# Optimization experiments

Hardware: AMD Instinct MI355X
Metric: run time of the kernel (lower is better)

The kernel has to match this reference:

```python
import jax, jax.numpy as jnp
import numpy as np

B, S, E, H = 4, 2048, 1024, 16
D = E // H  # head_dim = 64

def setup_inputs() -> dict:
    key = jax.random.key(0)
    k1, k2, k3, k4, k5 = jax.random.split(key, 5)
    x = jax.random.normal(k1, (B, S, E), dtype=jnp.float32)
    # causal mask, broadcast over batch and heads; mask==0 -> -inf
    mask = jnp.tril(jnp.ones((S, S), dtype=jnp.int32))[None, None, :, :]
    Wqkv = jax.random.normal(k2, (E, 3 * E), dtype=jnp.float32) * (1.0 / np.sqrt(E))
    bqkv = jax.random.normal(k3, (3 * E,), dtype=jnp.float32) * 0.02
    Wo = jax.random.normal(k4, (E, E), dtype=jnp.float32) * (1.0 / np.sqrt(E))
    bo = jax.random.normal(k5, (E,), dtype=jnp.float32) * 0.02
    return {"x": x, "mask": mask, "Wqkv": Wqkv, "bqkv": bqkv, "Wo": Wo, "bo": bo}

def reference(x, mask, Wqkv, bqkv, Wo, bo):
    b, s, e = x.shape
    scale = 1.0 / np.sqrt(D)
    qkv = x @ Wqkv + bqkv                      # [b,s,3e]
    qkv = qkv.reshape(b, s, H, 3 * D).transpose(0, 2, 1, 3)  # [b,h,s,3d]
    q, k, v = jnp.split(qkv, 3, axis=-1)       # each [b,h,s,d]
    scores = jnp.einsum('bnqd,bnkd->bnqk', q, k) * scale
    scores = jnp.where(mask == 0, -jnp.inf, scores)
    probs = jax.nn.softmax(scores, axis=-1)
    attn = jnp.einsum('bnqk,bnkd->bnqd', probs, v)  # [b,h,s,d]
    # Faithful to source: reshape (b,h,s,d) -> (b,s,e) WITHOUT transposing back
    attn = attn.reshape(b, s, e)
    return attn @ Wo + bo
```

## Files before the change

kernel.cpp:

```cpp
#include <hip/hip_runtime.h>

typedef __attribute__((ext_vector_type(8))) short bf16x8;
typedef __attribute__((ext_vector_type(4))) float f32x4;
typedef __attribute__((ext_vector_type(2))) unsigned int u32x2;
typedef __attribute__((ext_vector_type(4))) unsigned int u32x4;

#define MFMA16(a, b, c) __builtin_amdgcn_mfma_f32_16x16x32_bf16((a), (b), (c), 0, 0, 0)

#define S_LEN 2048
#define NHEAD 16
#define DHEAD 64
#define BH    64
#define MROWS 8192

__device__ __forceinline__ unsigned short f2bf(float f) {
  unsigned int u = __builtin_bit_cast(unsigned int, f);
  u += 0x7FFFu + ((u >> 16) & 1u);
  return (unsigned short)(u >> 16);
}

__device__ __forceinline__ void gl_lds16(const void* g, void* l) {
  __builtin_amdgcn_global_load_lds(
      (const __attribute__((address_space(1))) void*)g,
      (__attribute__((address_space(3))) void*)l, 16, 0, 0);
}

__device__ __forceinline__ unsigned int pkbf(float lo, float hi) {
  unsigned int ulo = __builtin_bit_cast(unsigned int, lo) + 0x8000u;
  unsigned int uhi = __builtin_bit_cast(unsigned int, hi) + 0x8000u;
  return __builtin_amdgcn_perm(uhi, ulo, 0x07060302u);
}

__global__ __launch_bounds__(256) void cast_bf16(const float* __restrict__ src,
                                                 unsigned short* __restrict__ dst, int n) {
  int i = (blockIdx.x * 256 + threadIdx.x) * 4;
  if (i + 3 < n) {
    f32x4 v = *(const f32x4*)(src + i);
    unsigned long long pk =
        (unsigned long long)f2bf(v[0]) |
        ((unsigned long long)f2bf(v[1]) << 16) |
        ((unsigned long long)f2bf(v[2]) << 32) |
        ((unsigned long long)f2bf(v[3]) << 48);
    *(unsigned long long*)(dst + i) = pk;
  }
}

__global__ __launch_bounds__(256) void transpose_cast(const float* __restrict__ src,
                                                      unsigned short* __restrict__ dst,
                                                      int R, int C) {
  __shared__ float tile[32][33];
  int c0 = blockIdx.x * 32, r0 = blockIdx.y * 32;
  int tx = threadIdx.x, ty = threadIdx.y;
  for (int i = 0; i < 32; i += 8)
    tile[ty + i][tx] = src[(size_t)(r0 + ty + i) * C + c0 + tx];
  __syncthreads();
  for (int i = 0; i < 32; i += 8)
    dst[(size_t)(c0 + ty + i) * R + r0 + tx] = f2bf(tile[tx][ty + i]);
}

__global__ __launch_bounds__(256) void transpose_cast_qkv(const float* __restrict__ src,
                                                          unsigned short* __restrict__ dst) {
  __shared__ float tile[32][33];
  int c0 = blockIdx.x * 32, r0 = blockIdx.y * 32;
  int tx = threadIdx.x, ty = threadIdx.y;
  for (int i = 0; i < 32; i += 8)
    tile[ty + i][tx] = src[(size_t)(r0 + ty + i) * 3072 + c0 + tx];
  __syncthreads();
  for (int i = 0; i < 32; i += 8) {
    int oc = c0 + ty + i;
    int h = oc / 192, rr = oc % 192;
    int nc = ((rr >> 6) << 10) + (h << 6) + (rr & 63);
    dst[(size_t)nc * 1024 + r0 + tx] = f2bf(tile[tx][ty + i]);
  }
}

#define GEMM_CORE(A_, Bt_)                                                              \
  __shared__ unsigned short As[128 * 32];                                               \
  __shared__ unsigned short Bs[128 * 32];                                               \
  const int tid = threadIdx.x;                                                          \
  const int w = tid >> 6, lane = tid & 63, l15 = lane & 15, quad = lane >> 4;           \
  const int wm = w >> 1, wn = w & 1;                                                    \
  const int col0 = blockIdx.x * 128, row0 = blockIdx.y * 128;                           \
  f32x4 acc[4][4] = {};                                                                 \
  for (int kt = 0; kt < 32; ++kt) {                                                     \
    const int k0 = kt * 32;                                                             \
    for (int p = 0; p < 2; ++p) {                                                       \
      int c = p * 256 + tid;                                                            \
      int m = c >> 2, k8 = (c & 3) * 8;                                                 \
      void* ldsA = (char*)As + (size_t)(p * 256 + (tid & 192)) * 16;                    \
      void* ldsB = (char*)Bs + (size_t)(p * 256 + (tid & 192)) * 16;                    \
      gl_lds16(A_ + (size_t)(row0 + m) * 1024 + k0 + k8, ldsA);                         \
      gl_lds16(Bt_ + (size_t)(col0 + m) * 1024 + k0 + k8, ldsB);                        \
    }                                                                                   \
    __syncthreads();                                                                    \
    bf16x8 af[4], bfr[4];                                                               \
    for (int i = 0; i < 4; ++i)                                                         \
      af[i] = *(const bf16x8*)&As[(wm * 64 + i * 16 + l15) * 32 + quad * 8];            \
    for (int j = 0; j < 4; ++j)                                                         \
      bfr[j] = *(const bf16x8*)&Bs[(wn * 64 + j * 16 + l15) * 32 + quad * 8];           \
    for (int i = 0; i < 4; ++i)                                                         \
      for (int j = 0; j < 4; ++j)                                                       \
        acc[i][j] = MFMA16(af[i], bfr[j], acc[i][j]);                                   \
    __syncthreads();                                                                    \
  }

__global__ __launch_bounds__(256) void gemm_qkv(const unsigned short* __restrict__ A,
                                                const unsigned short* __restrict__ Bt,
                                                const float* __restrict__ bias,
                                                unsigned short* __restrict__ Qb,
                                                unsigned short* __restrict__ Kb,
                                                unsigned short* __restrict__ Vtb) {
  __shared__ float Es[4][16][66];
  GEMM_CORE(A, Bt)
  const int bx = col0 >> 7;
  float bv[4];
  #pragma unroll
  for (int j = 0; j < 4; ++j) {
    int nc = col0 + wn * 64 + j * 16 + l15;
    int oc = ((nc >> 6) & 15) * 192 + (nc >> 10) * 64 + (nc & 63);
    bv[j] = bias[oc];
  }
  const float sc = (bx < 8) ? 0.18033688011112042f : 1.0f;
  const int b = row0 >> 11;
  const int srow0 = (row0 & 2047) + wm * 64;
  const int h = ((col0 + wn * 64) >> 6) & 15;
  float (*Ew)[66] = Es[w];

  if (bx < 16) {
    const int lr = lane >> 2, ch2 = lane & 3, d0 = ch2 * 16;
    unsigned short* base = (bx < 8 ? Qb : Kb) + ((size_t)(b * 16 + h) * 2048) * 64;
    for (int i = 0; i < 4; ++i) {
      #pragma unroll
      for (int j = 0; j < 4; ++j)
        #pragma unroll
        for (int r = 0; r < 4; ++r)
          Ew[quad * 4 + r][j * 16 + l15] = (acc[i][j][r] + bv[j]) * sc;
      float v[16];
      #pragma unroll
      for (int c = 0; c < 4; ++c)
        *(f32x4*)&v[4 * c] = *(const f32x4*)&Ew[lr][d0 + 4 * c];
      u32x4 pk0 = {pkbf(v[0], v[1]), pkbf(v[2], v[3]), pkbf(v[4], v[5]), pkbf(v[6], v[7])};
      u32x4 pk1 = {pkbf(v[8], v[9]), pkbf(v[10], v[11]), pkbf(v[12], v[13]), pkbf(v[14], v[15])};
      unsigned short* dst = base + (size_t)(srow0 + i * 16 + lr) * 64 + d0;
      *(u32x4*)dst = pk0;
      *(u32x4*)(dst + 8) = pk1;
    }
  } else {
    const int d = lane;
    unsigned short* base = Vtb + ((size_t)(b * 16 + h) * 64 + d) * 2048;
    for (int i = 0; i < 4; ++i) {
      #pragma unroll
      for (int j = 0; j < 4; ++j)
        #pragma unroll
        for (int r = 0; r < 4; ++r)
          Ew[quad * 4 + r][j * 16 + l15] = acc[i][j][r] + bv[j];
      float e[16];
      #pragma unroll
      for (int k = 0; k < 16; ++k) e[k] = Ew[k][d];
      u32x4 pk0 = {pkbf(e[0], e[1]), pkbf(e[2], e[3]), pkbf(e[4], e[5]), pkbf(e[6], e[7])};
      u32x4 pk1 = {pkbf(e[8], e[9]), pkbf(e[10], e[11]), pkbf(e[12], e[13]), pkbf(e[14], e[15])};
      unsigned short* dst = base + srow0 + i * 16;
      *(u32x4*)dst = pk0;
      *(u32x4*)(dst + 8) = pk1;
    }
  }
}

__global__ __launch_bounds__(256) void gemm_out(const unsigned short* __restrict__ A,
                                                const unsigned short* __restrict__ Bt,
                                                const float* __restrict__ bias,
                                                float* __restrict__ out) {
  GEMM_CORE(A, Bt)
  for (int i = 0; i < 4; ++i) {
    int grow = row0 + wm * 64 + i * 16 + quad * 4;
    for (int j = 0; j < 4; ++j) {
      int gcol = col0 + wn * 64 + j * 16 + l15;
      float bvv = bias[gcol];
      for (int r = 0; r < 4; ++r)
        out[(size_t)(grow + r) * 1024 + gcol] = acc[i][j][r] + bvv;
    }
  }
}

__global__ __launch_bounds__(256) void attn_kernel(const unsigned short* __restrict__ Qb,
                                                   const unsigned short* __restrict__ Kb,
                                                   const unsigned short* __restrict__ Vtb,
                                                   unsigned short* __restrict__ attnout) {
  __shared__ unsigned short K0[64 * 32], K1[64 * 32];
  __shared__ unsigned short V0[64 * 32], V1[64 * 32];
  __shared__ unsigned short P0[4][4][512], P1[4][4][512];
  __shared__ float Lbc[4][64];

  const int tid = threadIdx.x;
  const int w = tid >> 6, lane = tid & 63, l15 = lane & 15, quad = lane >> 4;
  const int i2 = blockIdx.x >> 6;
  const int jj = ((i2 & 1) << 1) | ((i2 >> 1) & 1);
  const int qt = (i2 & 4) ? jj : 7 - jj;
  const int bh = blockIdx.x & 63;
  const int q0w = qt * 256 + w * 64;

  const unsigned short* Qg = Qb + (size_t)bh * S_LEN * DHEAD;
  const unsigned short* Kg = Kb + (size_t)bh * S_LEN * DHEAD;
  const unsigned short* Vg = Vtb + (size_t)bh * DHEAD * S_LEN;

  bf16x8 qf[4][2];
  #pragma unroll
  for (int sub = 0; sub < 4; ++sub) {
    const unsigned short* p = Qg + (size_t)(q0w + sub * 16 + l15) * DHEAD + quad * 8;
    qf[sub][0] = *(const bf16x8*)p;
    qf[sub][1] = *(const bf16x8*)(p + 32);
  }

  const int srow = tid >> 2, sc8 = (tid & 3) * 8;
  const unsigned short* kgb = Kg + srow * 64 + sc8;
  const unsigned short* vgb = Vg + (size_t)srow * S_LEN + sc8;
  const int wKo = srow * 32 + sc8;

  const int psw = (l15 & 3) ^ ((l15 >> 2) & 3);
  const int pw0 = l15 * 32 + (((quad >> 1) ^ psw) << 3) + ((quad & 1) << 2);
  const int pw1 = l15 * 32 + ((((quad >> 1) + 2) ^ psw) << 3) + ((quad & 1) << 2);
  const int pro = l15 * 32 + ((quad ^ psw) << 3);
  const int kvo = l15 * 32 + quad * 8;

  f32x4 oacc[4][4] = {};
  float lacc[4] = {0.f, 0.f, 0.f, 0.f};

  const int ktdiag = 4 * qt;
  const int nkt = ktdiag + 4;

  bf16x8 kr0 = *(const bf16x8*)kgb, kr1 = *(const bf16x8*)(kgb + 32);
  bf16x8 vr0 = *(const bf16x8*)vgb, vr1 = *(const bf16x8*)(vgb + 32);

  for (int kt = 0; kt < nkt; ++kt) {
    *(bf16x8*)&K0[wKo] = kr0;  *(bf16x8*)&K1[wKo] = kr1;
    *(bf16x8*)&V0[wKo] = vr0;  *(bf16x8*)&V1[wKo] = vr1;
    __syncthreads();
    if (kt + 1 < nkt) {
      const unsigned short* kp = kgb + (kt + 1) * 4096;
      const unsigned short* vp = vgb + (kt + 1) * 64;
      kr0 = *(const bf16x8*)kp;  kr1 = *(const bf16x8*)(kp + 32);
      vr0 = *(const bf16x8*)vp;  vr1 = *(const bf16x8*)(vp + 32);
    }

    const int t = kt - ktdiag;
    const bool act = (t < 0) || (w >= t);

    if (act) {
      if (t < 0) {
        #pragma unroll
        for (int jk = 0; jk < 4; ++jk) {
          bf16x8 kf0 = *(const bf16x8*)&K0[jk * 512 + kvo];
          bf16x8 kf1 = *(const bf16x8*)&K1[jk * 512 + kvo];
          #pragma unroll
          for (int sub = 0; sub < 4; ++sub) {
            f32x4 z = {};
            z = MFMA16(kf0, qf[sub][0], z);
            z = MFMA16(kf1, qf[sub][1], z);
            float e0 = __builtin_amdgcn_exp2f(z[0]);
            float e1 = __builtin_amdgcn_exp2f(z[1]);
            float e2 = __builtin_amdgcn_exp2f(z[2]);
            float e3 = __builtin_amdgcn_exp2f(z[3]);
            lacc[sub] += (e0 + e1) + (e2 + e3);
            unsigned short* pd = (jk < 2) ? P0[w][sub] : P1[w][sub];
            *(u32x2*)&pd[(jk & 1) ? pw1 : pw0] = (u32x2){pkbf(e0, e1), pkbf(e2, e3)};
          }
        }
      } else {
        const bool dg = (t == w);
        #pragma unroll
        for (int jk = 0; jk < 4; ++jk) {
          bf16x8 kf0 = *(const bf16x8*)&K0[jk * 512 + kvo];
          bf16x8 kf1 = *(const bf16x8*)&K1[jk * 512 + kvo];
          #pragma unroll
          for (int sub = 0; sub < 4; ++sub) {
            unsigned short* pd = (jk < 2) ? P0[w][sub] : P1[w][sub];
            unsigned int* dst = (unsigned int*)&pd[(jk & 1) ? pw1 : pw0];
            if (dg && jk > sub) { *(u32x2*)dst = (u32x2){0u, 0u}; continue; }
            f32x4 z = {};
            z = MFMA16(kf0, qf[sub][0], z);
            z = MFMA16(kf1, qf[sub][1], z);
            if (dg && jk == sub) {
              #pragma unroll
              for (int r = 0; r < 4; ++r)
                if (quad * 4 + r > l15) z[r] = -3e38f;
            }
            float e0 = __builtin_amdgcn_exp2f(z[0]);
            float e1 = __builtin_amdgcn_exp2f(z[1]);
            float e2 = __builtin_amdgcn_exp2f(z[2]);
            float e3 = __builtin_amdgcn_exp2f(z[3]);
            lacc[sub] += (e0 + e1) + (e2 + e3);
            *(u32x2*)dst = (u32x2){pkbf(e0, e1), pkbf(e2, e3)};
          }
        }
      }

      bf16x8 pf[4][2];
      #pragma unroll
      for (int sub = 0; sub < 4; ++sub) {
        pf[sub][0] = *(const bf16x8*)&P0[w][sub][pro];
        pf[sub][1] = *(const bf16x8*)&P1[w][sub][pro];
      }
      #pragma unroll
      for (int dt = 0; dt < 4; ++dt) {
        bf16x8 vb0 = *(const bf16x8*)&V0[dt * 512 + kvo];
        bf16x8 vb1 = *(const bf16x8*)&V1[dt * 512 + kvo];
        #pragma unroll
        for (int sub = 0; sub < 4; ++sub) {
          oacc[sub][dt] = MFMA16(pf[sub][0], vb0, oacc[sub][dt]);
          oacc[sub][dt] = MFMA16(pf[sub][1], vb1, oacc[sub][dt]);
        }
      }
    }
    __syncthreads();
  }

  #pragma unroll
  for (int sub = 0; sub < 4; ++sub) {
    float l = lacc[sub];
    l += __shfl_xor(l, 16);
    l += __shfl_xor(l, 32);
    if (quad == 0) Lbc[w][sub * 16 + l15] = l;
  }
  #pragma unroll
  for (int sub = 0; sub < 4; ++sub) {
    f32x4 l4 = *(const f32x4*)&Lbc[w][sub * 16 + quad * 4];
    int qbase = q0w + sub * 16 + quad * 4;
    unsigned short* dst = attnout + ((size_t)bh * S_LEN + qbase) * DHEAD;
    #pragma unroll
    for (int r = 0; r < 4; ++r) {
      float inv = __builtin_amdgcn_rcpf(l4[r]);
      #pragma unroll
      for (int dt = 0; dt < 4; ++dt)
        dst[(size_t)r * DHEAD + dt * 16 + l15] = f2bf(oacc[sub][dt][r] * inv);
    }
  }
}

extern "C" void kernel_launch(void* const* d_in, const int* in_sizes, int n_in,
                              void* d_out, int out_size, void* d_ws, size_t ws_size,
                              hipStream_t stream) {
  const float* x    = (const float*)d_in[0];
  const float* Wqkv = (const float*)d_in[2];
  const float* bqkv = (const float*)d_in[3];
  const float* Wo   = (const float*)d_in[4];
  const float* bo   = (const float*)d_in[5];
  float* out = (float*)d_out;

  char* ws = (char*)d_ws;
  unsigned short* Xbf   = (unsigned short*)(ws);
  unsigned short* WqkvT = (unsigned short*)(ws + 16777216);
  unsigned short* WoT   = (unsigned short*)(ws + 23068672);
  unsigned short* Qb    = (unsigned short*)(ws + 25165824);
  unsigned short* Kb    = (unsigned short*)(ws + 41943040);
  unsigned short* Vtb   = (unsigned short*)(ws + 58720256);
  unsigned short* Attn  = (unsigned short*)(ws + 75497472);

  cast_bf16<<<8192, 256, 0, stream>>>(x, Xbf, MROWS * 1024);
  transpose_cast_qkv<<<dim3(96, 32), dim3(32, 8), 0, stream>>>(Wqkv, WqkvT);
  transpose_cast<<<dim3(32, 32), dim3(32, 8), 0, stream>>>(Wo, WoT, 1024, 1024);
  gemm_qkv<<<dim3(24, 64), 256, 0, stream>>>(Xbf, WqkvT, bqkv, Qb, Kb, Vtb);
  attn_kernel<<<512, 256, 0, stream>>>(Qb, Kb, Vtb, Attn);
  gemm_out<<<dim3(8, 64), 256, 0, stream>>>(Attn, WoT, bo, out);
}
```

Baseline: 266.4 us.

## Rewrite QKV GEMM with 256x256 tiles, double-buffered async LDS staging, swizzling

Replaces the QKV projection GEMM with a 512-thread, 256x256-tile kernel. It double-buffers the global-to-LDS loads across K tiles, with explicit vmcnt/lgkmcnt waits, barriers and raised MFMA priority, so loads overlap the matrix math. The LDS layout is XOR-swizzled to avoid bank conflicts, and the grid is remapped to a 1D grid of 384 blocks with a block-index permutation for better L2 reuse. This adds 128KB of LDS per block and relies on hand-tuned wait counts, which trades occupancy and fragility for higher MFMA utilisation in the dominant GEMM.

```diff
diff --git a/kernel.cpp b/kernel.cpp
--- a/kernel.cpp
+++ b/kernel.cpp
@@ -104,15 +104,155 @@
     __syncthreads();                                                                    \
   }
 
-__global__ __launch_bounds__(256) void gemm_qkv(const unsigned short* __restrict__ A,
-                                                const unsigned short* __restrict__ Bt,
-                                                const float* __restrict__ bias,
-                                                unsigned short* __restrict__ Qb,
-                                                unsigned short* __restrict__ Kb,
-                                                unsigned short* __restrict__ Vtb) {
-  __shared__ float Es[4][16][66];
-  GEMM_CORE(A, Bt)
-  const int bx = col0 >> 7;
+
+#define VM6 asm volatile("s_waitcnt vmcnt(6)" ::: "memory")
+#define VM0 asm volatile("s_waitcnt vmcnt(0)" ::: "memory")
+#define LGKM0 asm volatile("s_waitcnt lgkmcnt(0)" ::: "memory")
+#define BAR __builtin_amdgcn_s_barrier()
+
+#define STAGE_A(KT, H)                                                           \
+  do {                                                                           \
+    char* lb_ = SHB + (((KT) & 1) * 65536 + (H) * 16384) + stgo;                 \
+    const unsigned short* gs_ = a_src + (KT) * 64 + (H) * 32;                    \
+    gl_lds16(gs_, lb_);                                                          \
+    gl_lds16(gs_ + 131072, lb_ + 8192);                                          \
+  } while (0)
+#define STAGE_B(KT, H)                                                           \
+  do {                                                                           \
+    char* lb_ = SHB + (((KT) & 1) * 65536 + 32768 + (H) * 16384) + stgo;         \
+    const unsigned short* gs_ = b_src + (KT) * 64 + (H) * 32;                    \
+    gl_lds16(gs_, lb_);                                                          \
+    gl_lds16(gs_ + 131072, lb_ + 8192);                                          \
+  } while (0)
+
+#define MFMA_BLOCK(MH)                                                           \
+  __builtin_amdgcn_s_setprio(1);                                                 \
+  acc[(MH)*4+0][0] = MFMA16(af0, bq0, acc[(MH)*4+0][0]);                         \
+  acc[(MH)*4+0][1] = MFMA16(af0, bq1, acc[(MH)*4+0][1]);                         \
+  acc[(MH)*4+0][2] = MFMA16(af0, bq2, acc[(MH)*4+0][2]);                         \
+  acc[(MH)*4+0][3] = MFMA16(af0, bq3, acc[(MH)*4+0][3]);                         \
+  acc[(MH)*4+1][0] = MFMA16(af1, bq0, acc[(MH)*4+1][0]);                         \
+  acc[(MH)*4+1][1] = MFMA16(af1, bq1, acc[(MH)*4+1][1]);                         \
+  acc[(MH)*4+1][2] = MFMA16(af1, bq2, acc[(MH)*4+1][2]);                         \
+  acc[(MH)*4+1][3] = MFMA16(af1, bq3, acc[(MH)*4+1][3]);                         \
+  acc[(MH)*4+2][0] = MFMA16(af2, bq0, acc[(MH)*4+2][0]);                         \
+  acc[(MH)*4+2][1] = MFMA16(af2, bq1, acc[(MH)*4+2][1]);                         \
+  acc[(MH)*4+2][2] = MFMA16(af2, bq2, acc[(MH)*4+2][2]);                         \
+  acc[(MH)*4+2][3] = MFMA16(af2, bq3, acc[(MH)*4+2][3]);                         \
+  acc[(MH)*4+3][0] = MFMA16(af3, bq0, acc[(MH)*4+3][0]);                         \
+  acc[(MH)*4+3][1] = MFMA16(af3, bq1, acc[(MH)*4+3][1]);                         \
+  acc[(MH)*4+3][2] = MFMA16(af3, bq2, acc[(MH)*4+3][2]);                         \
+  acc[(MH)*4+3][3] = MFMA16(af3, bq3, acc[(MH)*4+3][3]);                         \
+  __builtin_amdgcn_s_setprio(0)
+
+#define KTILE(BUF, JT, G0, G2, VMW)                                              \
+  {                                                                              \
+    {                                                    \
+      const char* Ah_ = SHB + (BUF) * 65536;                                     \
+      const char* Bh_ = SHB + (BUF) * 65536 + 32768;                             \
+      bf16x8 af0 = *(const bf16x8*)(Ah_ + abase);                                \
+      bf16x8 af1 = *(const bf16x8*)(Ah_ + abase + 1024);                         \
+      bf16x8 af2 = *(const bf16x8*)(Ah_ + abase + 2048);                         \
+      bf16x8 af3 = *(const bf16x8*)(Ah_ + abase + 3072);                         \
+      bq0 = *(const bf16x8*)(Bh_ + bbase);                                       \
+      bq1 = *(const bf16x8*)(Bh_ + bbase + 1024);                                \
+      bq2 = *(const bf16x8*)(Bh_ + bbase + 2048);                                \
+      bq3 = *(const bf16x8*)(Bh_ + bbase + 3072);                                \
+      if (G0) STAGE_B((JT) + 1, 1);                                              \
+      BAR;                                                                       \
+      LGKM0;                                                                     \
+      MFMA_BLOCK(0);                                                             \
+      BAR;                                                                       \
+    }                                                                            \
+    {                                                    \
+      const char* Ah_ = SHB + (BUF) * 65536;                                     \
+      bf16x8 af0 = *(const bf16x8*)(Ah_ + abase + 4096);                         \
+      bf16x8 af1 = *(const bf16x8*)(Ah_ + abase + 5120);                         \
+      bf16x8 af2 = *(const bf16x8*)(Ah_ + abase + 6144);                         \
+      bf16x8 af3 = *(const bf16x8*)(Ah_ + abase + 7168);                         \
+      BAR;                                                                       \
+      if (G2) STAGE_A((JT) + 2, 0);                                              \
+      LGKM0;                                                                     \
+      MFMA_BLOCK(1);                                                             \
+      BAR;                                                                       \
+    }                                                                            \
+    {                                                    \
+      const char* Ah_ = SHB + (BUF) * 65536 + 16384;                             \
+      const char* Bh_ = SHB + (BUF) * 65536 + 32768 + 16384;                     \
+      bf16x8 af0 = *(const bf16x8*)(Ah_ + abase);                                \
+      bf16x8 af1 = *(const bf16x8*)(Ah_ + abase + 1024);                         \
+      bf16x8 af2 = *(const bf16x8*)(Ah_ + abase + 2048);                         \
+      bf16x8 af3 = *(const bf16x8*)(Ah_ + abase + 3072);                         \
+      bq0 = *(const bf16x8*)(Bh_ + bbase);                                       \
+      bq1 = *(const bf16x8*)(Bh_ + bbase + 1024);                                \
+      bq2 = *(const bf16x8*)(Bh_ + bbase + 2048);                                \
+      bq3 = *(const bf16x8*)(Bh_ + bbase + 3072);                                \
+      if (G2) STAGE_B((JT) + 2, 0);                                              \
+      BAR;                                                                       \
+      LGKM0;                                                                     \
+      MFMA_BLOCK(0);                                                             \
+      BAR;                                                                       \
+    }                                                                            \
+    {                                                    \
+      const char* Ah_ = SHB + (BUF) * 65536 + 16384;                             \
+      bf16x8 af0 = *(const bf16x8*)(Ah_ + abase + 4096);                         \
+      bf16x8 af1 = *(const bf16x8*)(Ah_ + abase + 5120);                         \
+      bf16x8 af2 = *(const bf16x8*)(Ah_ + abase + 6144);                         \
+      bf16x8 af3 = *(const bf16x8*)(Ah_ + abase + 7168);                         \
+      BAR;                                                                       \
+      if (G2) STAGE_A((JT) + 2, 1);                                              \
+      LGKM0;                                                                     \
+      MFMA_BLOCK(1);                                                             \
+      VMW;                                                                       \
+      BAR;                                                                       \
+    }                                                                            \
+  }
+
+__global__ __launch_bounds__(512, 2) void gemm_qkv(const unsigned short* __restrict__ A,
+                                                   const unsigned short* __restrict__ Bt,
+                                                   const float* __restrict__ bias,
+                                                   unsigned short* __restrict__ Qb,
+                                                   unsigned short* __restrict__ Kb,
+                                                   unsigned short* __restrict__ Vtb) {
+  __shared__ unsigned short SH[65536];
+  char* SHB = (char*)SH;
+  const int tid = threadIdx.x;
+  const int w = tid >> 6, lane = tid & 63, l15 = lane & 15, quad = lane >> 4;
+  const int wm = w >> 2, wn = w & 3;
+  const int g = ((blockIdx.x & 7) * 48) + (blockIdx.x >> 3);
+  const int bx = g % 12, by = g / 12;
+  const int col0 = bx << 8, row0 = by << 8;
+
+  const int qa = quad ^ ((l15 >> 1) & 3);
+  const int abase = (wm * 128 + l15) * 64 + qa * 16;
+  const int bbase = (wn * 64 + l15) * 64 + qa * 16;
+
+  const int qsw = (tid & 3) ^ ((tid >> 3) & 3);
+  const unsigned short* a_src = A + (size_t)(row0 + (tid >> 2)) * 1024 + qsw * 8;
+  const unsigned short* b_src = Bt + (size_t)(col0 + (tid >> 2)) * 1024 + qsw * 8;
+  const int stgo = (tid & ~63) * 16;
+
+  f32x4 acc[8][4] = {};
+  bf16x8 bq0, bq1, bq2, bq3;
+
+  STAGE_A(0, 0); STAGE_B(0, 0); STAGE_A(0, 1); STAGE_B(0, 1);
+  STAGE_A(1, 0); STAGE_B(1, 0); STAGE_A(1, 1);
+  VM6;
+  BAR;
+
+  #pragma unroll 1
+  for (int jj = 0; jj < 8; ++jj) {
+    const int j0 = jj * 2;
+    const bool more = (jj < 7);
+    KTILE(0, j0, 1, more, { if (more) VM6; else VM0; })
+    KTILE(1, j0 + 1, more, more, { if (more) VM6; })
+  }
+  __syncthreads();
+
+  const int which = col0 >> 10;
+  const int h = ((col0 + wn * 64) >> 6) & 15;
+  const int b = row0 >> 11;
+  const int srow0 = (row0 & 2047) + wm * 128;
   float bv[4];
   #pragma unroll
   for (int j = 0; j < 4; ++j) {
@@ -120,46 +260,45 @@
     int oc = ((nc >> 6) & 15) * 192 + (nc >> 10) * 64 + (nc & 63);
     bv[j] = bias[oc];
   }
-  const float sc = (bx < 8) ? 0.18033688011112042f : 1.0f;
-  const int b = row0 >> 11;
-  const int srow0 = (row0 & 2047) + wm * 64;
-  const int h = ((col0 + wn * 64) >> 6) & 15;
-  float (*Ew)[66] = Es[w];
-
-  if (bx < 16) {
-    const int lr = lane >> 2, ch2 = lane & 3, d0 = ch2 * 16;
-    unsigned short* base = (bx < 8 ? Qb : Kb) + ((size_t)(b * 16 + h) * 2048) * 64;
-    for (int i = 0; i < 4; ++i) {
+  float* Ew = (float*)SHB + w * 1072;
+
+  if (which < 2) {
+    const float sc = (which == 0) ? 0.18033688011112042f : 1.0f;
+    const int lr = lane >> 2, d0 = (lane & 3) * 16;
+    unsigned short* base = (which == 0 ? Qb : Kb) + ((size_t)(b * 16 + h) * 2048 + srow0) * 64;
+    #pragma unroll
+    for (int i = 0; i < 8; ++i) {
       #pragma unroll
       for (int j = 0; j < 4; ++j)
         #pragma unroll
         for (int r = 0; r < 4; ++r)
-          Ew[quad * 4 + r][j * 16 + l15] = (acc[i][j][r] + bv[j]) * sc;
+          Ew[(quad * 4 + r) * 66 + j * 16 + l15] = (acc[i][j][r] + bv[j]) * sc;
       float v[16];
       #pragma unroll
       for (int c = 0; c < 4; ++c)
-        *(f32x4*)&v[4 * c] = *(const f32x4*)&Ew[lr][d0 + 4 * c];
+        *(f32x4*)&v[4 * c] = *(const f32x4*)&Ew[lr * 66 + d0 + 4 * c];
       u32x4 pk0 = {pkbf(v[0], v[1]), pkbf(v[2], v[3]), pkbf(v[4], v[5]), pkbf(v[6], v[7])};
       u32x4 pk1 = {pkbf(v[8], v[9]), pkbf(v[10], v[11]), pkbf(v[12], v[13]), pkbf(v[14], v[15])};
-      unsigned short* dst = base + (size_t)(srow0 + i * 16 + lr) * 64 + d0;
+      unsigned short* dst = base + (size_t)(i * 16 + lr) * 64 + d0;
       *(u32x4*)dst = pk0;
       *(u32x4*)(dst + 8) = pk1;
     }
   } else {
     const int d = lane;
-    unsigned short* base = Vtb + ((size_t)(b * 16 + h) * 64 + d) * 2048;
-    for (int i = 0; i < 4; ++i) {
+    unsigned short* base = Vtb + ((size_t)(b * 16 + h) * 64 + d) * 2048 + srow0;
+    #pragma unroll
+    for (int i = 0; i < 8; ++i) {
       #pragma unroll
       for (int j = 0; j < 4; ++j)
         #pragma unroll
         for (int r = 0; r < 4; ++r)
-          Ew[quad * 4 + r][j * 16 + l15] = acc[i][j][r] + bv[j];
+          Ew[(quad * 4 + r) * 66 + j * 16 + l15] = acc[i][j][r] + bv[j];
       float e[16];
       #pragma unroll
-      for (int k = 0; k < 16; ++k) e[k] = Ew[k][d];
+      for (int k = 0; k < 16; ++k) e[k] = Ew[k * 66 + d];
       u32x4 pk0 = {pkbf(e[0], e[1]), pkbf(e[2], e[3]), pkbf(e[4], e[5]), pkbf(e[6], e[7])};
       u32x4 pk1 = {pkbf(e[8], e[9]), pkbf(e[10], e[11]), pkbf(e[12], e[13]), pkbf(e[14], e[15])};
-      unsigned short* dst = base + srow0 + i * 16;
+      unsigned short* dst = base + i * 16;
       *(u32x4*)dst = pk0;
       *(u32x4*)(dst + 8) = pk1;
     }
@@ -358,7 +497,7 @@
   cast_bf16<<<8192, 256, 0, stream>>>(x, Xbf, MROWS * 1024);
   transpose_cast_qkv<<<dim3(96, 32), dim3(32, 8), 0, stream>>>(Wqkv, WqkvT);
   transpose_cast<<<dim3(32, 32), dim3(32, 8), 0, stream>>>(Wo, WoT, 1024, 1024);
-  gemm_qkv<<<dim3(24, 64), 256, 0, stream>>>(Xbf, WqkvT, bqkv, Qb, Kb, Vtb);
+  gemm_qkv<<<384, 512, 0, stream>>>(Xbf, WqkvT, bqkv, Qb, Kb, Vtb);
   attn_kernel<<<512, 256, 0, stream>>>(Qb, Kb, Vtb, Attn);
   gemm_out<<<dim3(8, 64), 256, 0, stream>>>(Attn, WoT, bo, out);
 }
```

New measurement: 271.5 us. About the same (+1.9%).

## Rewrite QKV GEMM as 256x256 tile, double-buffered, software-pipelined kernel

Applied to the files above, without the earlier changes.

Replaces the simple 128x128 QKV projection GEMM with a 512-thread, 256x256-tile kernel. It double-buffers K=64 slabs in 128KB of LDS with direct global-to-LDS loads, interleaves the loads with MFMA blocks using explicit vmcnt waits, barriers and setprio, swizzles the LDS layout to avoid bank conflicts, and remaps the block index for L2 locality. The goal is to hide memory latency and raise MFMA utilization in the largest GEMM. The cost is high register pressure and only one block per CU because of the LDS use. The epilogue reuses the staging LDS.

```diff
diff --git a/kernel.cpp b/kernel.cpp
--- a/kernel.cpp
+++ b/kernel.cpp
@@ -101,18 +101,138 @@
     for (int i = 0; i < 4; ++i)                                                         \
       for (int j = 0; j < 4; ++j)                                                       \
         acc[i][j] = MFMA16(af[i], bfr[j], acc[i][j]);                                   \
+    for (int __z = 0; __z < 1; ++__z) ;                                                 \
     __syncthreads();                                                                    \
   }
 
-__global__ __launch_bounds__(256) void gemm_qkv(const unsigned short* __restrict__ A,
-                                                const unsigned short* __restrict__ Bt,
-                                                const float* __restrict__ bias,
-                                                unsigned short* __restrict__ Qb,
-                                                unsigned short* __restrict__ Kb,
-                                                unsigned short* __restrict__ Vtb) {
-  __shared__ float Es[4][16][66];
-  GEMM_CORE(A, Bt)
-  const int bx = col0 >> 7;
+
+#define VM8 asm volatile("s_waitcnt vmcnt(8)" ::: "memory")
+#define VM6 asm volatile("s_waitcnt vmcnt(6)" ::: "memory")
+#define VM4 asm volatile("s_waitcnt vmcnt(4)" ::: "memory")
+#define VM0 asm volatile("s_waitcnt vmcnt(0)" ::: "memory")
+#define VMNOP ((void)0)
+#define BAR __builtin_amdgcn_s_barrier()
+#define SB  __builtin_amdgcn_sched_barrier(0)
+
+#define STAGE_A(KT, H)                                                           \
+  do {                                                                           \
+    char* lb_ = SHB + (((KT) & 1) * 65536 + (H) * 16384) + stgo;                 \
+    const unsigned short* gs_ = a_src + (KT) * 64 + (H) * 32;                    \
+    gl_lds16(gs_, lb_);                                                          \
+    gl_lds16(gs_ + 131072, lb_ + 8192);                                          \
+  } while (0)
+#define STAGE_B(KT, H)                                                           \
+  do {                                                                           \
+    char* lb_ = SHB + (((KT) & 1) * 65536 + 32768 + (H) * 16384) + stgo;         \
+    const unsigned short* gs_ = b_src + (KT) * 64 + (H) * 32;                    \
+    gl_lds16(gs_, lb_);                                                          \
+    gl_lds16(gs_ + 131072, lb_ + 8192);                                          \
+  } while (0)
+
+#define MFMA_BLK(A0,A1,A2,A3, B0,B1,B2,B3, MH)                                   \
+  __builtin_amdgcn_s_setprio(1);                                                 \
+  acc[(MH)*4+0][0] = MFMA16(A0, B0, acc[(MH)*4+0][0]);                           \
+  acc[(MH)*4+0][1] = MFMA16(A0, B1, acc[(MH)*4+0][1]);                           \
+  acc[(MH)*4+0][2] = MFMA16(A0, B2, acc[(MH)*4+0][2]);                           \
+  acc[(MH)*4+0][3] = MFMA16(A0, B3, acc[(MH)*4+0][3]);                           \
+  acc[(MH)*4+1][0] = MFMA16(A1, B0, acc[(MH)*4+1][0]);                           \
+  acc[(MH)*4+1][1] = MFMA16(A1, B1, acc[(MH)*4+1][1]);                           \
+  acc[(MH)*4+1][2] = MFMA16(A1, B2, acc[(MH)*4+1][2]);                           \
+  acc[(MH)*4+1][3] = MFMA16(A1, B3, acc[(MH)*4+1][3]);                           \
+  acc[(MH)*4+2][0] = MFMA16(A2, B0, acc[(MH)*4+2][0]);                           \
+  acc[(MH)*4+2][1] = MFMA16(A2, B1, acc[(MH)*4+2][1]);                           \
+  acc[(MH)*4+2][2] = MFMA16(A2, B2, acc[(MH)*4+2][2]);                           \
+  acc[(MH)*4+2][3] = MFMA16(A2, B3, acc[(MH)*4+2][3]);                           \
+  acc[(MH)*4+3][0] = MFMA16(A3, B0, acc[(MH)*4+3][0]);                           \
+  acc[(MH)*4+3][1] = MFMA16(A3, B1, acc[(MH)*4+3][1]);                           \
+  acc[(MH)*4+3][2] = MFMA16(A3, B2, acc[(MH)*4+3][2]);                           \
+  acc[(MH)*4+3][3] = MFMA16(A3, B3, acc[(MH)*4+3][3]);                           \
+  __builtin_amdgcn_s_setprio(0)
+
+#define RD4(D0,D1,D2,D3, P)                                                      \
+  D0 = *(const bf16x8*)((P));                                                    \
+  D1 = *(const bf16x8*)((P) + 1024);                                             \
+  D2 = *(const bf16x8*)((P) + 2048);                                             \
+  D3 = *(const bf16x8*)((P) + 3072)
+
+#define KT1(BUF, JT, G1, G2, RDN, VMA_, VMB_)                                    \
+  {              \
+    if (G1) { STAGE_A((JT)+1, 1); STAGE_B((JT)+1, 1); }                          \
+    MFMA_BLK(afA0,afA1,afA2,afA3, bqA0,bqA1,bqA2,bqA3, 0);                       \
+    RD4(afB0,afB1,afB2,afB3, SHB + (BUF)*65536 + abase + 4096);                  \
+    VMA_; SB; BAR; SB;                                                           \
+  }                                                                              \
+  {                 \
+    MFMA_BLK(afB0,afB1,afB2,afB3, bqA0,bqA1,bqA2,bqA3, 1);                       \
+    RD4(afA0,afA1,afA2,afA3, SHB + (BUF)*65536 + 16384 + abase);                 \
+    RD4(bqB0,bqB1,bqB2,bqB3, SHB + (BUF)*65536 + 49152 + bbase);                 \
+    SB; BAR; SB;                                                                 \
+  }                                                                              \
+  {            \
+    if (G2) STAGE_A((JT)+2, 0);                                                  \
+    MFMA_BLK(afA0,afA1,afA2,afA3, bqB0,bqB1,bqB2,bqB3, 0);                       \
+    RD4(afB0,afB1,afB2,afB3, SHB + (BUF)*65536 + 16384 + abase + 4096);          \
+    VMB_; SB; BAR; SB;                                                           \
+  }                                                                              \
+  {               \
+    if (G2) STAGE_B((JT)+2, 0);                                                  \
+    MFMA_BLK(afB0,afB1,afB2,afB3, bqB0,bqB1,bqB2,bqB3, 1);                       \
+    if (RDN) {                                                                   \
+      RD4(afA0,afA1,afA2,afA3, SHB + (1-(BUF))*65536 + abase);                   \
+      RD4(bqA0,bqA1,bqA2,bqA3, SHB + (1-(BUF))*65536 + 32768 + bbase);           \
+    }                                                                            \
+    SB; BAR; SB;                                                                 \
+  }
+
+__global__ __launch_bounds__(512, 2) void gemm_qkv(const unsigned short* __restrict__ A,
+                                                   const unsigned short* __restrict__ Bt,
+                                                   const float* __restrict__ bias,
+                                                   unsigned short* __restrict__ Qb,
+                                                   unsigned short* __restrict__ Kb,
+                                                   unsigned short* __restrict__ Vtb) {
+  __shared__ unsigned short SH[65536];
+  char* SHB = (char*)SH;
+  const int tid = threadIdx.x;
+  const int w = tid >> 6, lane = tid & 63, l15 = lane & 15, quad = lane >> 4;
+  const int wm = w >> 2, wn = w & 3;
+  const int g = ((blockIdx.x & 7) * 48) + (blockIdx.x >> 3);
+  const int bx = g % 12, by = g / 12;
+  const int col0 = bx << 8, row0 = by << 8;
+
+  const int qa = quad ^ ((l15 >> 1) & 3);
+  const int abase = (wm * 128 + l15) * 64 + qa * 16;
+  const int bbase = (wn * 64 + l15) * 64 + qa * 16;
+
+  const int qsw = (tid & 3) ^ ((tid >> 3) & 3);
+  const unsigned short* a_src = A + (size_t)(row0 + (tid >> 2)) * 1024 + qsw * 8;
+  const unsigned short* b_src = Bt + (size_t)(col0 + (tid >> 2)) * 1024 + qsw * 8;
+  const int stgo = (tid & ~63) * 16;
+
+  f32x4 acc[8][4] = {};
+  bf16x8 afA0, afA1, afA2, afA3, afB0, afB1, afB2, afB3;
+  bf16x8 bqA0, bqA1, bqA2, bqA3, bqB0, bqB1, bqB2, bqB3;
+
+  STAGE_A(0, 0); STAGE_B(0, 0); STAGE_A(0, 1); STAGE_B(0, 1);
+  STAGE_A(1, 0); STAGE_B(1, 0);
+  VM8; SB; BAR; SB;
+  RD4(afA0, afA1, afA2, afA3, SHB + abase);
+  RD4(bqA0, bqA1, bqA2, bqA3, SHB + 32768 + bbase);
+
+  #pragma unroll 1
+  for (int jj = 0; jj < 7; ++jj) {
+    const int j0 = 2 * jj;
+    KT1(0, j0,     1, 1, 1, VM8, VM6)
+    KT1(1, j0 + 1, 1, 1, 1, VM8, VM6)
+  }
+  KT1(0, 14, 1, 0, 1, VM8, VM4)
+  KT1(1, 15, 0, 0, 0, VM0, VMNOP)
+  VM0;
+  __syncthreads();
+
+  const int which = col0 >> 10;
+  const int h = ((col0 + wn * 64) >> 6) & 15;
+  const int b = row0 >> 11;
+  const int srow0 = (row0 & 2047) + wm * 128;
   float bv[4];
   #pragma unroll
   for (int j = 0; j < 4; ++j) {
@@ -120,46 +240,45 @@
     int oc = ((nc >> 6) & 15) * 192 + (nc >> 10) * 64 + (nc & 63);
     bv[j] = bias[oc];
   }
-  const float sc = (bx < 8) ? 0.18033688011112042f : 1.0f;
-  const int b = row0 >> 11;
-  const int srow0 = (row0 & 2047) + wm * 64;
-  const int h = ((col0 + wn * 64) >> 6) & 15;
-  float (*Ew)[66] = Es[w];
-
-  if (bx < 16) {
-    const int lr = lane >> 2, ch2 = lane & 3, d0 = ch2 * 16;
-    unsigned short* base = (bx < 8 ? Qb : Kb) + ((size_t)(b * 16 + h) * 2048) * 64;
-    for (int i = 0; i < 4; ++i) {
+  float* Ew = (float*)SHB + w * 1072;
+
+  if (which < 2) {
+    const float sc = (which == 0) ? 0.18033688011112042f : 1.0f;
+    const int lr = lane >> 2, d0 = (lane & 3) * 16;
+    unsigned short* base = (which == 0 ? Qb : Kb) + ((size_t)(b * 16 + h) * 2048 + srow0) * 64;
+    #pragma unroll
+    for (int i = 0; i < 8; ++i) {
       #pragma unroll
       for (int j = 0; j < 4; ++j)
         #pragma unroll
         for (int r = 0; r < 4; ++r)
-          Ew[quad * 4 + r][j * 16 + l15] = (acc[i][j][r] + bv[j]) * sc;
+          Ew[(quad * 4 + r) * 66 + j * 16 + l15] = (acc[i][j][r] + bv[j]) * sc;
       float v[16];
       #pragma unroll
       for (int c = 0; c < 4; ++c)
-        *(f32x4*)&v[4 * c] = *(const f32x4*)&Ew[lr][d0 + 4 * c];
+        *(f32x4*)&v[4 * c] = *(const f32x4*)&Ew[lr * 66 + d0 + 4 * c];
       u32x4 pk0 = {pkbf(v[0], v[1]), pkbf(v[2], v[3]), pkbf(v[4], v[5]), pkbf(v[6], v[7])};
       u32x4 pk1 = {pkbf(v[8], v[9]), pkbf(v[10], v[11]), pkbf(v[12], v[13]), pkbf(v[14], v[15])};
-      unsigned short* dst = base + (size_t)(srow0 + i * 16 + lr) * 64 + d0;
+      unsigned short* dst = base + (size_t)(i * 16 + lr) * 64 + d0;
       *(u32x4*)dst = pk0;
       *(u32x4*)(dst + 8) = pk1;
     }
   } else {
     const int d = lane;
-    unsigned short* base = Vtb + ((size_t)(b * 16 + h) * 64 + d) * 2048;
-    for (int i = 0; i < 4; ++i) {
+    unsigned short* base = Vtb + ((size_t)(b * 16 + h) * 64 + d) * 2048 + srow0;
+    #pragma unroll
+    for (int i = 0; i < 8; ++i) {
       #pragma unroll
       for (int j = 0; j < 4; ++j)
         #pragma unroll
         for (int r = 0; r < 4; ++r)
-          Ew[quad * 4 + r][j * 16 + l15] = acc[i][j][r] + bv[j];
+          Ew[(quad * 4 + r) * 66 + j * 16 + l15] = acc[i][j][r] + bv[j];
       float e[16];
       #pragma unroll
-      for (int k = 0; k < 16; ++k) e[k] = Ew[k][d];
+      for (int k = 0; k < 16; ++k) e[k] = Ew[k * 66 + d];
       u32x4 pk0 = {pkbf(e[0], e[1]), pkbf(e[2], e[3]), pkbf(e[4], e[5]), pkbf(e[6], e[7])};
       u32x4 pk1 = {pkbf(e[8], e[9]), pkbf(e[10], e[11]), pkbf(e[12], e[13]), pkbf(e[14], e[15])};
-      unsigned short* dst = base + srow0 + i * 16;
+      unsigned short* dst = base + i * 16;
       *(u32x4*)dst = pk0;
       *(u32x4*)(dst + 8) = pk1;
     }
@@ -358,7 +477,7 @@
   cast_bf16<<<8192, 256, 0, stream>>>(x, Xbf, MROWS * 1024);
   transpose_cast_qkv<<<dim3(96, 32), dim3(32, 8), 0, stream>>>(Wqkv, WqkvT);
   transpose_cast<<<dim3(32, 32), dim3(32, 8), 0, stream>>>(Wo, WoT, 1024, 1024);
-  gemm_qkv<<<dim3(24, 64), 256, 0, stream>>>(Xbf, WqkvT, bqkv, Qb, Kb, Vtb);
+  gemm_qkv<<<384, 512, 0, stream>>>(Xbf, WqkvT, bqkv, Qb, Kb, Vtb);
   attn_kernel<<<512, 256, 0, stream>>>(Qb, Kb, Vtb, Attn);
   gemm_out<<<dim3(8, 64), 256, 0, stream>>>(Attn, WoT, bo, out);
 }
```

Result: no change. 269.5 us (+1.2%).

## Rewrite QKV GEMM with 512-thread tiles, double-buffered LDS pipeline and swizzle

Applied to the files above, without the earlier changes.

The QKV projection GEMM moves from 128x128 tiles with 256 threads to 128x256 tiles with 512 threads (8 waves). The main loop becomes a hand-scheduled double-buffered pipeline: async global-to-LDS loads overlap MFMA work, with explicit vmcnt waits, sched_group_barrier interleaving and setprio. It also adds an XOR swizzle on the LDS layout to avoid bank conflicts and remaps block indices to group tiles by XCD. The aim is to hide load latency and cut barrier stalls in the largest GEMM, at the cost of complex manual scheduling and higher register and LDS pressure.

```diff
diff --git a/kernel.cpp b/kernel.cpp
--- a/kernel.cpp
+++ b/kernel.cpp
@@ -104,15 +104,126 @@
     __syncthreads();                                                                    \
   }
 
-__global__ __launch_bounds__(256) void gemm_qkv(const unsigned short* __restrict__ A,
-                                                const unsigned short* __restrict__ Bt,
-                                                const float* __restrict__ bias,
-                                                unsigned short* __restrict__ Qb,
-                                                unsigned short* __restrict__ Kb,
-                                                unsigned short* __restrict__ Vtb) {
-  __shared__ float Es[4][16][66];
-  GEMM_CORE(A, Bt)
-  const int bx = col0 >> 7;
+
+#define VM3 asm volatile("s_waitcnt vmcnt(3)" ::: "memory")
+#define VM0 asm volatile("s_waitcnt vmcnt(0)" ::: "memory")
+#define BAR __builtin_amdgcn_s_barrier()
+#define SB  __builtin_amdgcn_sched_barrier(0)
+#define SGB_G(m, n) __builtin_amdgcn_sched_group_barrier((m), (n), 0)
+
+#define SGBPAT                                                                   \
+  SGB_G(0x70, 3);                                                                \
+  SGB_G(0x8, 2); SGB_G(0x100, 1); SGB_G(0x8, 2); SGB_G(0x100, 1);                \
+  SGB_G(0x8, 2); SGB_G(0x100, 1); SGB_G(0x8, 2); SGB_G(0x100, 1);                \
+  SGB_G(0x8, 2); SGB_G(0x100, 1); SGB_G(0x8, 2); SGB_G(0x100, 1);                \
+  SGB_G(0x8, 2); SGB_G(0x100, 1); SGB_G(0x8, 2); SGB_G(0x100, 1)
+
+#define STAGE3(T, KH, BUF)                                                       \
+  do {                                                                           \
+    const unsigned short* ga_ = a_src + (T) * 64 + (KH) * 32;                    \
+    const unsigned short* gb_ = b_src + (T) * 64 + (KH) * 32;                    \
+    char* la_ = SHB + (BUF) * 49152 + (KH) * 8192 + stgo;                        \
+    char* lb_ = SHB + (BUF) * 49152 + 16384 + (KH) * 16384 + stgo;               \
+    gl_lds16(ga_, la_);                                                          \
+    gl_lds16(gb_, lb_);                                                          \
+    gl_lds16(gb_ + 131072, lb_ + 8192);                                          \
+  } while (0)
+
+#define RDSET(S, BUF, KH)                                                        \
+  do {                                                                           \
+    const char* Ab_ = SHB + (BUF) * 49152 + (KH) * 8192 + abase;                 \
+    const char* Bb_ = SHB + (BUF) * 49152 + 16384 + (KH) * 16384 + bbase;        \
+    af##S##0 = *(const bf16x8*)(Ab_);                                            \
+    af##S##1 = *(const bf16x8*)(Ab_ + 1024);                                     \
+    af##S##2 = *(const bf16x8*)(Ab_ + 2048);                                     \
+    af##S##3 = *(const bf16x8*)(Ab_ + 3072);                                     \
+    bq##S##0 = *(const bf16x8*)(Bb_);                                            \
+    bq##S##1 = *(const bf16x8*)(Bb_ + 1024);                                     \
+    bq##S##2 = *(const bf16x8*)(Bb_ + 2048);                                     \
+    bq##S##3 = *(const bf16x8*)(Bb_ + 3072);                                     \
+  } while (0)
+
+#define MFMA16S(S)                                                               \
+  acc[0][0] = MFMA16(af##S##0, bq##S##0, acc[0][0]);                             \
+  acc[0][1] = MFMA16(af##S##0, bq##S##1, acc[0][1]);                             \
+  acc[0][2] = MFMA16(af##S##0, bq##S##2, acc[0][2]);                             \
+  acc[0][3] = MFMA16(af##S##0, bq##S##3, acc[0][3]);                             \
+  acc[1][0] = MFMA16(af##S##1, bq##S##0, acc[1][0]);                             \
+  acc[1][1] = MFMA16(af##S##1, bq##S##1, acc[1][1]);                             \
+  acc[1][2] = MFMA16(af##S##1, bq##S##2, acc[1][2]);                             \
+  acc[1][3] = MFMA16(af##S##1, bq##S##3, acc[1][3]);                             \
+  acc[2][0] = MFMA16(af##S##2, bq##S##0, acc[2][0]);                             \
+  acc[2][1] = MFMA16(af##S##2, bq##S##1, acc[2][1]);                             \
+  acc[2][2] = MFMA16(af##S##2, bq##S##2, acc[2][2]);                             \
+  acc[2][3] = MFMA16(af##S##2, bq##S##3, acc[2][3]);                             \
+  acc[3][0] = MFMA16(af##S##3, bq##S##0, acc[3][0]);                             \
+  acc[3][1] = MFMA16(af##S##3, bq##S##1, acc[3][1]);                             \
+  acc[3][2] = MFMA16(af##S##3, bq##S##2, acc[3][2]);                             \
+  acc[3][3] = MFMA16(af##S##3, bq##S##3, acc[3][3])
+
+#define WND(SP, STG_, VM_, RD_)                                                  \
+  {                                                                              \
+    STG_;                                                                        \
+    __builtin_amdgcn_s_setprio(1);                                               \
+    MFMA16S(SP);                                                                 \
+    RD_;                                                                         \
+    __builtin_amdgcn_s_setprio(0);                                               \
+    SGBPAT;                                                                      \
+    VM_; SB; BAR; SB;                                                            \
+  }
+
+__global__ __launch_bounds__(512, 2) void gemm_qkv(const unsigned short* __restrict__ A,
+                                                   const unsigned short* __restrict__ Bt,
+                                                   const float* __restrict__ bias,
+                                                   unsigned short* __restrict__ Qb,
+                                                   unsigned short* __restrict__ Kb,
+                                                   unsigned short* __restrict__ Vtb) {
+  __shared__ unsigned short SH[49152];
+  char* SHB = (char*)SH;
+  const int tid = threadIdx.x;
+  const int w = tid >> 6, lane = tid & 63, l15 = lane & 15, quad = lane >> 4;
+  const int wm = w >> 2, wn = w & 3;
+  const int g = ((blockIdx.x & 7) * 96) + (blockIdx.x >> 3);
+  const int bx = g % 12, by = g / 12;
+  const int col0 = bx << 8, row0 = by << 7;
+
+  const int qa = quad ^ ((l15 >> 1) & 3);
+  const int abase = (wm * 64 + l15) * 64 + qa * 16;
+  const int bbase = (wn * 64 + l15) * 64 + qa * 16;
+
+  const int qsw = (tid & 3) ^ ((tid >> 3) & 3);
+  const unsigned short* a_src = A + (size_t)(row0 + (tid >> 2)) * 1024 + qsw * 8;
+  const unsigned short* b_src = Bt + (size_t)(col0 + (tid >> 2)) * 1024 + qsw * 8;
+  const int stgo = (tid & ~63) * 16;
+
+  f32x4 acc[4][4] = {};
+  bf16x8 afA0, afA1, afA2, afA3, bqA0, bqA1, bqA2, bqA3;
+  bf16x8 afB0, afB1, afB2, afB3, bqB0, bqB1, bqB2, bqB3;
+
+  STAGE3(0, 0, 0); STAGE3(0, 1, 0); STAGE3(1, 0, 1);
+  VM3; SB; BAR; SB;
+  RDSET(A, 0, 0);
+
+  #pragma unroll 1
+  for (int jj = 0; jj < 7; ++jj) {
+    const int J0 = 2 * jj;
+    WND(A, STAGE3(J0 + 1, 1, 1), VM3, RDSET(B, 0, 1))
+    WND(B, STAGE3(J0 + 2, 0, 0), VM3, RDSET(A, 1, 0))
+    WND(A, STAGE3(J0 + 2, 1, 0), VM3, RDSET(B, 1, 1))
+    WND(B, STAGE3(J0 + 3, 0, 1), VM3, RDSET(A, 0, 0))
+  }
+  WND(A, STAGE3(15, 1, 1), VM3, RDSET(B, 0, 1))
+  WND(B, (void)0, VM0, RDSET(A, 1, 0))
+  WND(A, (void)0, (void)0, RDSET(B, 1, 1))
+  __builtin_amdgcn_s_setprio(1);
+  MFMA16S(B);
+  __builtin_amdgcn_s_setprio(0);
+  __syncthreads();
+
+  const int which = col0 >> 10;
+  const int h = ((col0 + wn * 64) >> 6) & 15;
+  const int b = row0 >> 11;
+  const int srow0 = (row0 & 2047) + wm * 64;
   float bv[4];
   #pragma unroll
   for (int j = 0; j < 4; ++j) {
@@ -120,46 +231,45 @@
     int oc = ((nc >> 6) & 15) * 192 + (nc >> 10) * 64 + (nc & 63);
     bv[j] = bias[oc];
   }
-  const float sc = (bx < 8) ? 0.18033688011112042f : 1.0f;
-  const int b = row0 >> 11;
-  const int srow0 = (row0 & 2047) + wm * 64;
-  const int h = ((col0 + wn * 64) >> 6) & 15;
-  float (*Ew)[66] = Es[w];
-
-  if (bx < 16) {
-    const int lr = lane >> 2, ch2 = lane & 3, d0 = ch2 * 16;
-    unsigned short* base = (bx < 8 ? Qb : Kb) + ((size_t)(b * 16 + h) * 2048) * 64;
+  float* Ew = (float*)SHB + w * 1072;
+
+  if (which < 2) {
+    const float sc = (which == 0) ? 0.18033688011112042f : 1.0f;
+    const int lr = lane >> 2, d0 = (lane & 3) * 16;
+    unsigned short* base = (which == 0 ? Qb : Kb) + ((size_t)(b * 16 + h) * 2048 + srow0) * 64;
+    #pragma unroll
     for (int i = 0; i < 4; ++i) {
       #pragma unroll
       for (int j = 0; j < 4; ++j)
         #pragma unroll
         for (int r = 0; r < 4; ++r)
-          Ew[quad * 4 + r][j * 16 + l15] = (acc[i][j][r] + bv[j]) * sc;
+          Ew[(quad * 4 + r) * 66 + j * 16 + l15] = (acc[i][j][r] + bv[j]) * sc;
       float v[16];
       #pragma unroll
       for (int c = 0; c < 4; ++c)
-        *(f32x4*)&v[4 * c] = *(const f32x4*)&Ew[lr][d0 + 4 * c];
+        *(f32x4*)&v[4 * c] = *(const f32x4*)&Ew[lr * 66 + d0 + 4 * c];
       u32x4 pk0 = {pkbf(v[0], v[1]), pkbf(v[2], v[3]), pkbf(v[4], v[5]), pkbf(v[6], v[7])};
       u32x4 pk1 = {pkbf(v[8], v[9]), pkbf(v[10], v[11]), pkbf(v[12], v[13]), pkbf(v[14], v[15])};
-      unsigned short* dst = base + (size_t)(srow0 + i * 16 + lr) * 64 + d0;
+      unsigned short* dst = base + (size_t)(i * 16 + lr) * 64 + d0;
       *(u32x4*)dst = pk0;
       *(u32x4*)(dst + 8) = pk1;
     }
   } else {
     const int d = lane;
-    unsigned short* base = Vtb + ((size_t)(b * 16 + h) * 64 + d) * 2048;
+    unsigned short* base = Vtb + ((size_t)(b * 16 + h) * 64 + d) * 2048 + srow0;
+    #pragma unroll
     for (int i = 0; i < 4; ++i) {
       #pragma unroll
       for (int j = 0; j < 4; ++j)
         #pragma unroll
         for (int r = 0; r < 4; ++r)
-          Ew[quad * 4 + r][j * 16 + l15] = acc[i][j][r] + bv[j];
+          Ew[(quad * 4 + r) * 66 + j * 16 + l15] = acc[i][j][r] + bv[j];
       float e[16];
       #pragma unroll
-      for (int k = 0; k < 16; ++k) e[k] = Ew[k][d];
+      for (int k = 0; k < 16; ++k) e[k] = Ew[k * 66 + d];
       u32x4 pk0 = {pkbf(e[0], e[1]), pkbf(e[2], e[3]), pkbf(e[4], e[5]), pkbf(e[6], e[7])};
       u32x4 pk1 = {pkbf(e[8], e[9]), pkbf(e[10], e[11]), pkbf(e[12], e[13]), pkbf(e[14], e[15])};
-      unsigned short* dst = base + srow0 + i * 16;
+      unsigned short* dst = base + i * 16;
       *(u32x4*)dst = pk0;
       *(u32x4*)(dst + 8) = pk1;
     }
@@ -358,7 +468,7 @@
   cast_bf16<<<8192, 256, 0, stream>>>(x, Xbf, MROWS * 1024);
   transpose_cast_qkv<<<dim3(96, 32), dim3(32, 8), 0, stream>>>(Wqkv, WqkvT);
   transpose_cast<<<dim3(32, 32), dim3(32, 8), 0, stream>>>(Wo, WoT, 1024, 1024);
-  gemm_qkv<<<dim3(24, 64), 256, 0, stream>>>(Xbf, WqkvT, bqkv, Qb, Kb, Vtb);
+  gemm_qkv<<<768, 512, 0, stream>>>(Xbf, WqkvT, bqkv, Qb, Kb, Vtb);
   attn_kernel<<<512, 256, 0, stream>>>(Qb, Kb, Vtb, Attn);
   gemm_out<<<dim3(8, 64), 256, 0, stream>>>(Attn, WoT, bo, out);
 }
```

After: 275.2 us. 3.3% more time.
